# Performance work log

Hardware: AMD Instinct MI355X
Metric: run time of the kernel (lower is better)

Reference implementation:

```python
import jax, jax.numpy as jnp
import numpy as np

D = 1024
H = 16

def setup_inputs() -> dict:
    key = jax.random.key(0)
    k1, k2, k3 = jax.random.split(key, 3)
    x = jax.random.normal(k1, (2, 2048, D), dtype=jnp.float32)
    # torch Linear weights: qkv (3d, d), proj (d, d); y = x @ W.T
    w_qkv = jax.random.normal(k2, (3 * D, D), dtype=jnp.float32) * (1.0 / np.sqrt(D))
    w_proj = jax.random.normal(k3, (D, D), dtype=jnp.float32) * (1.0 / np.sqrt(D))
    return {"x": x, "w_qkv": w_qkv, "w_proj": w_proj}

def reference(x, w_qkv, w_proj):
    B, T, C = x.shape
    hd = C // H  # head dim
    qkv = x @ w_qkv.T                     # [B,T,3C]
    q, k, v = jnp.split(qkv, 3, axis=-1)
    q = q.reshape(B, T, H, hd).transpose(0, 2, 1, 3)  # [B,H,T,hd]
    k = k.reshape(B, T, H, hd).transpose(0, 2, 1, 3)
    v = v.reshape(B, T, H, hd).transpose(0, 2, 1, 3)
    att = jnp.einsum('bhqd,bhkd->bhqk', q, k) * (hd ** -0.5)  # [B,H,T,T]
    mask = jnp.triu(jnp.ones((T, T), dtype=bool), 1)
    att = jnp.where(mask, jnp.float32(-1e9), att)
    att = jax.nn.softmax(att, axis=-1)
    y = jnp.einsum('bhqk,bhkd->bhqd', att, v)  # [B,H,T,hd]
    y = y.transpose(0, 2, 1, 3).reshape(B, T, C)
    return y @ w_proj.T
```

## Files before the change

### kernel.cpp

```cpp
#include <hip/hip_runtime.h>
#include <hip/hip_bf16.h>


typedef __bf16 bf16;
typedef __bf16 bf16x8 __attribute__((ext_vector_type(8)));
typedef __bf16 bf16x4 __attribute__((ext_vector_type(4)));
typedef float f32x4 __attribute__((ext_vector_type(4)));

__device__ __forceinline__ bf16 f2bf(float f) {
    unsigned u = __builtin_bit_cast(unsigned, f);
    u += 0x7fffu + ((u >> 16) & 1u);
    unsigned short h = (unsigned short)(u >> 16);
    return __builtin_bit_cast(bf16, h);
}

__device__ __forceinline__ unsigned pack2(float a, float b) {
    unsigned ua = __builtin_bit_cast(unsigned, a);
    unsigned ub = __builtin_bit_cast(unsigned, b);
    return (ua >> 16) | (ub & 0xFFFF0000u);
}

__device__ __forceinline__ bf16x8 ld8f(const float* p) {
    f32x4 a = *(const f32x4*)p;
    f32x4 b = *(const f32x4*)(p + 4);
    bf16x8 r;
#pragma unroll
    for (int i = 0; i < 4; i++) { r[i] = f2bf(a[i]); r[i + 4] = f2bf(b[i]); }
    return r;
}

__device__ __forceinline__ void st_out(bf16* p, float v)  { *p = f2bf(v); }
__device__ __forceinline__ void st_out(float* p, float v) { *p = v; }

__global__ __launch_bounds__(256) void cvt_bf16(const float* __restrict__ src,
                                                bf16* __restrict__ dst, int n) {
    int i = (blockIdx.x * 256 + threadIdx.x) * 8;
    if (i < n) *(bf16x8*)&dst[i] = ld8f(&src[i]);
}

__device__ __forceinline__ void glds16(const bf16* g, bf16* l) {
    __builtin_amdgcn_global_load_lds(
        (const __attribute__((address_space(1))) void*)g,
        (__attribute__((address_space(3))) void*)l, 16, 0, 0);
}

template <typename TC, int BN>
__global__ __launch_bounds__(256) void gemm_glds(const bf16* __restrict__ A, int lda, int aoff,
                                                 const bf16* __restrict__ W,
                                                 TC* __restrict__ C, int N, int K) {
    constexpr int NI = (BN == 128) ? 4 : 2;
    __shared__ bf16 sA[2][128 * 32];
    __shared__ bf16 sW[2][BN * 32];
    const int bm = blockIdx.x * 128, bn = blockIdx.y * BN;
    const int tid = threadIdx.x;
    const int wave = tid >> 6, lane = tid & 63;
    const int quad = lane >> 4, l16 = lane & 15;
    const int rbase = (BN == 128) ? (wave >> 1) * 64 : wave * 32;
    const int cbase = (BN == 128) ? (wave & 1) * 64 : 0;
    const int r16 = lane >> 2, cl = lane & 3;
    const int gch = cl ^ ((r16 >> 1) & 3);
    const int sl  = (l16 >> 1) & 3;

    auto stage = [&](int bufi, int k0) {
#pragma unroll
        for (int t = 0; t < 2; t++) {
            int row = wave * 32 + t * 16 + r16;
            glds16(&A[(size_t)(bm + row) * lda + aoff + k0 + gch * 8],
                   &sA[bufi][(wave * 32 + t * 16) * 32]);
        }
        if (BN == 128) {
#pragma unroll
            for (int t = 0; t < 2; t++) {
                int row = wave * 32 + t * 16 + r16;
                glds16(&W[(size_t)(bn + row) * K + k0 + gch * 8],
                       &sW[bufi][(wave * 32 + t * 16) * 32]);
            }
        } else {
            int row = wave * 16 + r16;
            glds16(&W[(size_t)(bn + row) * K + k0 + gch * 8], &sW[bufi][(wave * 16) * 32]);
        }
    };

    f32x4 acc[NI][4] = {};

    stage(0, 0);
    asm volatile("s_waitcnt vmcnt(0)" ::: "memory");
    __syncthreads();

    const int nsteps = K >> 5;
    for (int s = 0; s < nsteps; s++) {
        const int buf = s & 1;
        if (s + 1 < nsteps) stage(buf ^ 1, (s + 1) * 32);

        bf16x8 af[NI], bfr[4];
#pragma unroll
        for (int i = 0; i < NI; i++)
            af[i] = *(bf16x8*)&sA[buf][(rbase + i * 16 + l16) * 32 + (quad ^ sl) * 8];
#pragma unroll
        for (int j = 0; j < 4; j++)
            bfr[j] = *(bf16x8*)&sW[buf][(cbase + j * 16 + l16) * 32 + (quad ^ sl) * 8];
#pragma unroll
        for (int i = 0; i < NI; i++)
#pragma unroll
            for (int j = 0; j < 4; j++)
                acc[i][j] = __builtin_amdgcn_mfma_f32_16x16x32_bf16(
                    af[i], bfr[j], acc[i][j], 0, 0, 0);

        asm volatile("s_waitcnt vmcnt(0)" ::: "memory");
        __syncthreads();
    }

#pragma unroll
    for (int i = 0; i < NI; i++)
#pragma unroll
        for (int j = 0; j < 4; j++)
#pragma unroll
            for (int r = 0; r < 4; r++) {
                int row = bm + rbase + i * 16 + quad * 4 + r;
                int col = bn + cbase + j * 16 + l16;
                st_out(&C[(size_t)row * N + col], acc[i][j][r]);
            }
}

__global__ __launch_bounds__(256) void transpose_v(const bf16* __restrict__ qkv,
                                                   bf16* __restrict__ vt) {
    __shared__ bf16 s[64][72];
    const int tt = blockIdx.x;
    const int bh = blockIdx.y;
    const int b = bh >> 4, h = bh & 15;
    const int tid = threadIdx.x;

    for (int c = tid; c < 512; c += 256) {
        int t = c >> 3, dc = (c & 7) * 8;
        *(bf16x8*)&s[t][dc] =
            *(const bf16x8*)&qkv[((size_t)(b * 2048 + tt * 64 + t)) * 3072 + 2048 + h * 64 + dc];
    }
    __syncthreads();
    for (int c = tid; c < 512; c += 256) {
        int d = c >> 3, tc = (c & 7) * 8;
        bf16x8 o;
#pragma unroll
        for (int e = 0; e < 8; e++) o[e] = s[tc + e][d];
        *(bf16x8*)&vt[((size_t)bh * 64 + d) * 2048 + tt * 64 + tc] = o;
    }
}

__global__ __launch_bounds__(256, 2) void attn(bf16* __restrict__ qkv,
                                               const bf16* __restrict__ vt) {
    const int bh = blockIdx.x;
    const int y  = blockIdx.y;
    const int g  = (y < 8) ? (15 - y) : (y - 8);
    const int b = bh >> 4, h = bh & 15;
    const int tid  = threadIdx.x;
    const int wave = tid >> 6;
    const int lane = tid & 63;
    const int quad = lane >> 4, l16 = lane & 15;

    __shared__ bf16 sK[2][64 * 64];
    __shared__ bf16 sV[2][64 * 64];

    bf16* base = qkv + (size_t)b * 2048 * 3072;
    const bf16* vbh = vt + (size_t)bh * 64 * 2048;

    const int iq = g * 4 + wave;
    const int qb = iq * 32;
    const int kint = iq >> 1;
    const int ktmax = 2 * g + 1;
    const float SC = 0.125f * 1.44269504f;

    const int srow = lane >> 3;
    const int schk = (lane & 7) ^ srow;

    auto stage = [&](int bufi, int kt) {
#pragma unroll
        for (int u = 0; u < 2; u++) {
            int s = wave * 2 + u;
            glds16(&base[(size_t)(kt * 64 + s * 8 + srow) * 3072 + 1024 + h * 64 + schk * 8],
                   &sK[bufi][s * 512]);
            glds16(&vbh[(size_t)(s * 8 + srow) * 2048 + kt * 64 + schk * 8],
                   &sV[bufi][s * 512]);
        }
    };

    bf16x8 qa[2][2];
#pragma unroll
    for (int rt = 0; rt < 2; rt++)
#pragma unroll
        for (int c = 0; c < 2; c++)
            qa[rt][c] = *(const bf16x8*)&base[(size_t)(qb + rt * 16 + l16) * 3072 +
                                              h * 64 + c * 32 + quad * 8];

    f32x4 acc[2][4] = {};
    float lpart[2] = {0.0f, 0.0f};
    const int sw = l16 & 7;

    auto body = [&](int kt, bool tail, int bufi) {
        const bf16* K = sK[bufi];
        const bf16* V = sV[bufi];

        bf16x8 kb[4][2];
#pragma unroll
        for (int j = 0; j < 4; j++)
#pragma unroll
            for (int c = 0; c < 2; c++)
                kb[j][c] = *(const bf16x8*)&K[(j * 16 + l16) * 64 + ((c * 4 + quad) ^ sw) * 8];

        bf16x8 vb[4][2];
#pragma unroll
        for (int dt = 0; dt < 4; dt++)
#pragma unroll
            for (int c = 0; c < 2; c++) {
                const bf16* vr = &V[(dt * 16 + l16) * 64];
                union { bf16x4 h[2]; bf16x8 v; } u;
                u.h[0] = *(const bf16x4*)&vr[((4 * c +     (quad >> 1)) ^ sw) * 8 + (quad & 1) * 4];
                u.h[1] = *(const bf16x4*)&vr[((4 * c + 2 + (quad >> 1)) ^ sw) * 8 + (quad & 1) * 4];
                vb[dt][c] = u.v;
            }

        f32x4 S[2][4] = {};
#pragma unroll
        for (int j = 0; j < 4; j++)
#pragma unroll
            for (int rt = 0; rt < 2; rt++) {
                S[rt][j] = __builtin_amdgcn_mfma_f32_16x16x32_bf16(kb[j][0], qa[rt][0], S[rt][j], 0, 0, 0);
                S[rt][j] = __builtin_amdgcn_mfma_f32_16x16x32_bf16(kb[j][1], qa[rt][1], S[rt][j], 0, 0, 0);
            }

        unsigned pk[2][4][2];
#pragma unroll
        for (int rt = 0; rt < 2; rt++) {
            const int qg = qb + rt * 16 + l16;
#pragma unroll
            for (int j = 0; j < 4; j++) {
                float p[4];
#pragma unroll
                for (int r = 0; r < 4; r++) {
                    float pv = exp2f(S[rt][j][r] * SC - 8.0f);
                    if (tail) {
                        int kg = kt * 64 + j * 16 + quad * 4 + r;
                        pv = (kg > qg) ? 0.0f : pv;
                    }
                    p[r] = pv;
                }
                lpart[rt] += (p[0] + p[1]) + (p[2] + p[3]);
                pk[rt][j][0] = pack2(p[0], p[1]);
                pk[rt][j][1] = pack2(p[2], p[3]);
            }
        }

#pragma unroll
        for (int rt = 0; rt < 2; rt++)
#pragma unroll
            for (int c = 0; c < 2; c++) {
                union { unsigned u[4]; bf16x8 v; } pb;
                pb.u[0] = pk[rt][2 * c][0];
                pb.u[1] = pk[rt][2 * c][1];
                pb.u[2] = pk[rt][2 * c + 1][0];
                pb.u[3] = pk[rt][2 * c + 1][1];
#pragma unroll
                for (int dt = 0; dt < 4; dt++)
                    acc[rt][dt] = __builtin_amdgcn_mfma_f32_16x16x32_bf16(
                        vb[dt][c], pb.v, acc[rt][dt], 0, 0, 0);
            }
    };

    stage(0, 0);
    asm volatile("s_waitcnt vmcnt(0)" ::: "memory");
    __syncthreads();
    int buf = 0;
    for (int kt = 0; kt <= ktmax; kt++) {
        if (kt + 1 <= ktmax) stage(buf ^ 1, kt + 1);
        if (kt <= kint) body(kt, kt == kint, buf);
        asm volatile("s_waitcnt vmcnt(0)" ::: "memory");
        __syncthreads();
        buf ^= 1;
    }

#pragma unroll
    for (int rt = 0; rt < 2; rt++) {
        lpart[rt] += __shfl_xor(lpart[rt], 16);
        lpart[rt] += __shfl_xor(lpart[rt], 32);
    }

#pragma unroll
    for (int rt = 0; rt < 2; rt++) {
        float inv = 1.0f / lpart[rt];
        int row = qb + rt * 16 + l16;
#pragma unroll
        for (int dt = 0; dt < 4; dt++) {
            bf16x4 o;
#pragma unroll
            for (int r = 0; r < 4; r++) o[r] = f2bf(acc[rt][dt][r] * inv);
            *(bf16x4*)&base[(size_t)row * 3072 + 2048 + h * 64 + dt * 16 + quad * 4] = o;
        }
    }
}

extern "C" void kernel_launch(void* const* d_in, const int* in_sizes, int n_in,
                              void* d_out, int out_size, void* d_ws, size_t ws_size,
                              hipStream_t stream) {
    (void)out_size; (void)ws_size;
    const float *x = (const float*)d_in[0], *w_qkv = (const float*)d_in[1],
                *w_proj = (const float*)d_in[2];
    for (int i = 0; i < n_in; i++) {
        if (in_sizes[i] == 4194304) x = (const float*)d_in[i];
        else if (in_sizes[i] == 3145728) w_qkv = (const float*)d_in[i];
        else if (in_sizes[i] == 1048576) w_proj = (const float*)d_in[i];
    }

    float* out = (float*)d_out;
    bf16* xb   = (bf16*)d_out;
    bf16* qkv  = (bf16*)d_ws;
    bf16* r2   = qkv + (size_t)4096 * 3072;
    bf16* wqb  = r2;
    bf16* vt   = r2;
    bf16* wpb  = r2;

    cvt_bf16<<<dim3(2048), dim3(256), 0, stream>>>(x, xb, 4096 * 1024);
    cvt_bf16<<<dim3(1536), dim3(256), 0, stream>>>(w_qkv, wqb, 3072 * 1024);
    gemm_glds<bf16, 128><<<dim3(32, 24), dim3(256), 0, stream>>>(
        xb, 1024, 0, wqb, qkv, 3072, 1024);
    transpose_v<<<dim3(32, 32), dim3(256), 0, stream>>>(qkv, vt);
    attn<<<dim3(32, 16), dim3(256), 0, stream>>>(qkv, vt);
    cvt_bf16<<<dim3(512), dim3(256), 0, stream>>>(w_proj, wpb, 1024 * 1024);
    gemm_glds<float, 128><<<dim3(32, 8), dim3(256), 0, stream>>>(
        qkv, 3072, 2048, wpb, out, 1024, 1024);
}
```

Baseline: 202.1 us.

## Run attention as single-wave blocks loading K/V directly from global memory

Replaces the 4-wave attention block, which staged K and V tiles into double-buffered shared memory, with one-wave blocks of 32 query rows. Each wave reads its K and V fragments straight from global memory, with no LDS staging or barriers, and runs only the causal tiles it needs. The intent is to drop synchronisation and the idle staging iterations that waves with short causal ranges spent on the shared schedule, and to improve load balance with a finer grid. In exchange, K/V reuse across the waves of a block is lost, so global or L2 traffic rises and load latency is no longer overlapped by explicit prefetch.

Result: slower. 248.0 us (+22.8%).

```diff
diff --git a/kernel.cpp b/kernel.cpp
--- a/kernel.cpp
+++ b/kernel.cpp
@@ -145,42 +145,19 @@
     }
 }
 
-__global__ __launch_bounds__(256, 2) void attn(bf16* __restrict__ qkv,
-                                               const bf16* __restrict__ vt) {
+__global__ __launch_bounds__(64, 3) void attn(bf16* __restrict__ qkv,
+                                              const bf16* __restrict__ vt) {
     const int bh = blockIdx.x;
-    const int y  = blockIdx.y;
-    const int g  = (y < 8) ? (15 - y) : (y - 8);
+    const int i  = 63 - blockIdx.y;
     const int b = bh >> 4, h = bh & 15;
-    const int tid  = threadIdx.x;
-    const int wave = tid >> 6;
-    const int lane = tid & 63;
+    const int lane = threadIdx.x;
     const int quad = lane >> 4, l16 = lane & 15;
-
-    __shared__ bf16 sK[2][64 * 64];
-    __shared__ bf16 sV[2][64 * 64];
 
     bf16* base = qkv + (size_t)b * 2048 * 3072;
     const bf16* vbh = vt + (size_t)bh * 64 * 2048;
-
-    const int iq = g * 4 + wave;
-    const int qb = iq * 32;
-    const int kint = iq >> 1;
-    const int ktmax = 2 * g + 1;
+    const int qb = i * 32;
+    const int kint = i >> 1;
     const float SC = 0.125f * 1.44269504f;
-
-    const int srow = lane >> 3;
-    const int schk = (lane & 7) ^ srow;
-
-    auto stage = [&](int bufi, int kt) {
-#pragma unroll
-        for (int u = 0; u < 2; u++) {
-            int s = wave * 2 + u;
-            glds16(&base[(size_t)(kt * 64 + s * 8 + srow) * 3072 + 1024 + h * 64 + schk * 8],
-                   &sK[bufi][s * 512]);
-            glds16(&vbh[(size_t)(s * 8 + srow) * 2048 + kt * 64 + schk * 8],
-                   &sV[bufi][s * 512]);
-        }
-    };
 
     bf16x8 qa[2][2];
 #pragma unroll
@@ -192,30 +169,30 @@
 
     f32x4 acc[2][4] = {};
     float lpart[2] = {0.0f, 0.0f};
-    const int sw = l16 & 7;
-
-    auto body = [&](int kt, bool tail, int bufi) {
-        const bf16* K = sK[bufi];
-        const bf16* V = sV[bufi];
+
+    for (int kt = 0; kt <= kint; kt++) {
+        const bool tail = (kt == kint);
 
         bf16x8 kb[4][2];
 #pragma unroll
-        for (int j = 0; j < 4; j++)
-#pragma unroll
-            for (int c = 0; c < 2; c++)
-                kb[j][c] = *(const bf16x8*)&K[(j * 16 + l16) * 64 + ((c * 4 + quad) ^ sw) * 8];
+        for (int j = 0; j < 4; j++) {
+            const bf16* kr = &base[(size_t)(kt * 64 + j * 16 + l16) * 3072 + 1024 + h * 64];
+            kb[j][0] = *(const bf16x8*)&kr[quad * 8];
+            kb[j][1] = *(const bf16x8*)&kr[32 + quad * 8];
+        }
 
         bf16x8 vb[4][2];
 #pragma unroll
-        for (int dt = 0; dt < 4; dt++)
+        for (int dt = 0; dt < 4; dt++) {
+            const bf16* vr = &vbh[(size_t)(dt * 16 + l16) * 2048 + kt * 64 + quad * 4];
 #pragma unroll
             for (int c = 0; c < 2; c++) {
-                const bf16* vr = &V[(dt * 16 + l16) * 64];
-                union { bf16x4 h[2]; bf16x8 v; } u;
-                u.h[0] = *(const bf16x4*)&vr[((4 * c +     (quad >> 1)) ^ sw) * 8 + (quad & 1) * 4];
-                u.h[1] = *(const bf16x4*)&vr[((4 * c + 2 + (quad >> 1)) ^ sw) * 8 + (quad & 1) * 4];
+                union { bf16x4 h4[2]; bf16x8 v; } u;
+                u.h4[0] = *(const bf16x4*)&vr[c * 32];
+                u.h4[1] = *(const bf16x4*)&vr[c * 32 + 16];
                 vb[dt][c] = u.v;
             }
+        }
 
         f32x4 S[2][4] = {};
 #pragma unroll
@@ -262,18 +239,6 @@
                     acc[rt][dt] = __builtin_amdgcn_mfma_f32_16x16x32_bf16(
                         vb[dt][c], pb.v, acc[rt][dt], 0, 0, 0);
             }
-    };
-
-    stage(0, 0);
-    asm volatile("s_waitcnt vmcnt(0)" ::: "memory");
-    __syncthreads();
-    int buf = 0;
-    for (int kt = 0; kt <= ktmax; kt++) {
-        if (kt + 1 <= ktmax) stage(buf ^ 1, kt + 1);
-        if (kt <= kint) body(kt, kt == kint, buf);
-        asm volatile("s_waitcnt vmcnt(0)" ::: "memory");
-        __syncthreads();
-        buf ^= 1;
     }
 
 #pragma unroll
@@ -321,7 +286,7 @@
     gemm_glds<bf16, 128><<<dim3(32, 24), dim3(256), 0, stream>>>(
         xb, 1024, 0, wqb, qkv, 3072, 1024);
     transpose_v<<<dim3(32, 32), dim3(256), 0, stream>>>(qkv, vt);
-    attn<<<dim3(32, 16), dim3(256), 0, stream>>>(qkv, vt);
+    attn<<<dim3(32, 64), dim3(64), 0, stream>>>(qkv, vt);
     cvt_bf16<<<dim3(512), dim3(256), 0, stream>>>(w_proj, wpb, 1024 * 1024);
     gemm_glds<float, 128><<<dim3(32, 8), dim3(256), 0, stream>>>(
         qkv, 3072, 2048, wpb, out, 1024, 1024);
```
